# Kernel optimization log

Hardware: AMD Instinct MI355X
Metric: run time of the kernel (lower is better)

## Reference

```python
import jax, jax.numpy as jnp
import numpy as np

B, F, E = 1024, 1024, 256      # batch, flat_shape (mobilenet), embedding_size
L1, L2, L3 = 16, 8, 32         # level1 classes, level2 classes per branch, level3 classes per leaf
NE3 = L1 * L2                  # 128 leaf (level-3) classifier heads


def setup_inputs() -> dict:
    key = jax.random.key(0)
    ks = jax.random.split(key, 10)
    w = lambda k, shape: (jax.random.normal(k, shape, jnp.float32) * 0.02)
    return {
        "features_x": jax.random.normal(ks[0], (B, F), jnp.float32),
        "features_y": jax.random.normal(ks[1], (B, F), jnp.float32),
        # level-1 head: Linear(F->E, no bias) + LayerNorm + ReLU + Linear(E->L1)
        "l1_W1": w(ks[2], (F, E)),
        "l1_g": jnp.ones((E,), jnp.float32), "l1_b": jnp.zeros((E,), jnp.float32),
        "l1_W2": w(ks[3], (E, L1)), "l1_b2": jnp.zeros((L1,), jnp.float32),
        # level-2 heads (one per level-1 class), stacked on a leading expert axis
        "l2_W1": w(ks[4], (L1, F, E)),
        "l2_g": jnp.ones((L1, E), jnp.float32), "l2_b": jnp.zeros((L1, E), jnp.float32),
        "l2_W2": w(ks[5], (L1, E, L2)), "l2_b2": jnp.zeros((L1, L2), jnp.float32),
        # level-3 heads (flattened [level1][level2] -> NE3 experts)
        "l3_W1": w(ks[6], (NE3, F, E)),
        "l3_g": jnp.ones((NE3, E), jnp.float32), "l3_b": jnp.zeros((NE3, E), jnp.float32),
        "l3_W2": w(ks[7], (NE3, E, L3)), "l3_b2": jnp.zeros((NE3, L3), jnp.float32),
    }


def _ln(h, g, b, eps=1e-5):
    m = jnp.mean(h, axis=-1, keepdims=True)
    v = jnp.mean(jnp.square(h - m), axis=-1, keepdims=True)
    return (h - m) * jax.lax.rsqrt(v + eps) * g + b


def reference(features_x, features_y,
              l1_W1, l1_g, l1_b, l1_W2, l1_b2,
              l2_W1, l2_g, l2_b, l2_W2, l2_b2,
              l3_W1, l3_g, l3_b, l3_W2, l3_b2):
    # Dropout is identity in eval mode.
    x, y = features_x, features_y
    rows = jnp.arange(x.shape[0])

    # level 1: single head on x
    h1 = jax.nn.relu(_ln(x @ l1_W1, l1_g, l1_b))
    logits1 = h1 @ l1_W2 + l1_b2                                # [B, L1]
    idx1 = jnp.argmax(logits1, axis=-1)                         # argmax(softmax) == argmax

    # level 2: routed head on 0.6*x + 0.4*y; compute all L1 heads batched, gather selected
    ft = 0.6 * x + 0.4 * y
    h2 = jax.nn.relu(_ln(jnp.einsum('bf,efh->beh', ft, l2_W1), l2_g, l2_b))  # [B, L1, E]
    logits2_all = jnp.einsum('beh,ehc->bec', h2, l2_W2) + l2_b2              # [B, L1, L2]
    logits2 = logits2_all[rows, idx1]                                        # [B, L2]
    idx2 = jnp.argmax(logits2, axis=-1)

    # level 3: doubly-routed head on x; flat expert index = idx1*L2 + idx2
    eidx = idx1 * logits2.shape[-1] + idx2
    h3 = jax.nn.relu(_ln(jnp.einsum('bf,efh->beh', x, l3_W1), l3_g, l3_b))   # [B, NE3, E]
    logits3_all = jnp.einsum('beh,ehc->bec', h3, l3_W2) + l3_b2              # [B, NE3, L3]
    logits3 = logits3_all[rows, eidx]                                        # [B, L3]

    # uniform class counts => pad_sequence is a no-op
    return (logits1, logits2, logits3)
```

## Files before the change

### kernel.cpp

```cpp
#include <hip/hip_runtime.h>

#define B_    1024
#define F_    1024
#define E_    256
#define NL1   16
#define NL2   8
#define NL3   32
#define NE3_  128
#define CS1   4
#define CS    8
#define MAXCH2 160
#define MAXCH3 256
#define OUT2_OFF (B_ * NL1)
#define OUT3_OFF (B_ * (NL1 + NL2))

__device__ __forceinline__ float b2f(unsigned short u) {
    union { unsigned int i; float f; } v; v.i = ((unsigned int)u) << 16; return v.f;
}
__device__ __forceinline__ unsigned short f2b(float f) {
    union { float f; unsigned int i; } v; v.f = f;
    unsigned int x = v.i; x += 0x7fffu + ((x >> 16) & 1u);
    return (unsigned short)(x >> 16);
}

template<int R, int NC>
__device__ void head_chunk(
    const float* __restrict__ in,
    const void* W1v, const void* gv_, const void* bv_,
    const void* W2v, const void* b2v, int bf,
    float* part,
    float* hn,
    float* red,
    float* lg,
    int t)
{
    const int lane = t & 63;
    const int grp  = t >> 6;
    const int e0   = lane * 4;

    float acc[R][4];
    #pragma unroll
    for (int r = 0; r < R; ++r) { acc[r][0]=0.f; acc[r][1]=0.f; acc[r][2]=0.f; acc[r][3]=0.f; }

    const float* ing = in + grp * 256;

    if (bf) {
        const unsigned short* W = (const unsigned short*)W1v + (size_t)grp * 256 * E_;
        for (int f0 = 0; f0 < 256; f0 += 16) {
            ushort4 w[16];
            #pragma unroll
            for (int k = 0; k < 16; ++k)
                w[k] = *(const ushort4*)(W + (size_t)(f0 + k) * E_ + e0);
            #pragma unroll
            for (int q = 0; q < 4; ++q) {
                float4 xq[R];
                #pragma unroll
                for (int r = 0; r < R; ++r)
                    xq[r] = *(const float4*)(ing + r * F_ + f0 + q * 4);
                #pragma unroll
                for (int k2 = 0; k2 < 4; ++k2) {
                    ushort4 ww = w[q * 4 + k2];
                    float w0 = b2f(ww.x), w1 = b2f(ww.y), w2 = b2f(ww.z), w3 = b2f(ww.w);
                    #pragma unroll
                    for (int r = 0; r < R; ++r) {
                        float xv = (k2 == 0) ? xq[r].x : (k2 == 1) ? xq[r].y
                                 : (k2 == 2) ? xq[r].z : xq[r].w;
                        acc[r][0] += xv * w0; acc[r][1] += xv * w1;
                        acc[r][2] += xv * w2; acc[r][3] += xv * w3;
                    }
                }
            }
        }
    } else {
        const float* W = (const float*)W1v + (size_t)grp * 256 * E_;
        for (int f0 = 0; f0 < 256; f0 += 8) {
            float4 w[8];
            #pragma unroll
            for (int k = 0; k < 8; ++k)
                w[k] = *(const float4*)(W + (size_t)(f0 + k) * E_ + e0);
            #pragma unroll
            for (int q = 0; q < 2; ++q) {
                float4 xq[R];
                #pragma unroll
                for (int r = 0; r < R; ++r)
                    xq[r] = *(const float4*)(ing + r * F_ + f0 + q * 4);
                #pragma unroll
                for (int k2 = 0; k2 < 4; ++k2) {
                    float4 ww = w[q * 4 + k2];
                    #pragma unroll
                    for (int r = 0; r < R; ++r) {
                        float xv = (k2 == 0) ? xq[r].x : (k2 == 1) ? xq[r].y
                                 : (k2 == 2) ? xq[r].z : xq[r].w;
                        acc[r][0] += xv * ww.x; acc[r][1] += xv * ww.y;
                        acc[r][2] += xv * ww.z; acc[r][3] += xv * ww.w;
                    }
                }
            }
        }
    }

    #pragma unroll
    for (int r = 0; r < R; ++r) {
        part[(size_t)(grp * R + r) * E_ + e0 + 0] = acc[r][0];
        part[(size_t)(grp * R + r) * E_ + e0 + 1] = acc[r][1];
        part[(size_t)(grp * R + r) * E_ + e0 + 2] = acc[r][2];
        part[(size_t)(grp * R + r) * E_ + e0 + 3] = acc[r][3];
    }
    __syncthreads();

    float h[R];
    #pragma unroll
    for (int r = 0; r < R; ++r)
        h[r] = part[(0 * R + r) * E_ + t] + part[(1 * R + r) * E_ + t]
             + part[(2 * R + r) * E_ + t] + part[(3 * R + r) * E_ + t];

    #pragma unroll
    for (int r = 0; r < R; ++r) {
        float s = h[r], ss = h[r] * h[r];
        #pragma unroll
        for (int o = 32; o > 0; o >>= 1) { s += __shfl_xor(s, o); ss += __shfl_xor(ss, o); }
        if (lane == 0) { red[(grp * R + r) * 2 + 0] = s; red[(grp * R + r) * 2 + 1] = ss; }
    }
    __syncthreads();

    float gv, bv;
    if (bf) { gv = b2f(((const unsigned short*)gv_)[t]); bv = b2f(((const unsigned short*)bv_)[t]); }
    else    { gv = ((const float*)gv_)[t];               bv = ((const float*)bv_)[t]; }

    #pragma unroll
    for (int r = 0; r < R; ++r) {
        float S  = red[(0*R+r)*2] + red[(1*R+r)*2] + red[(2*R+r)*2] + red[(3*R+r)*2];
        float SS = red[(0*R+r)*2+1] + red[(1*R+r)*2+1] + red[(2*R+r)*2+1] + red[(3*R+r)*2+1];
        float m    = S * (1.0f / E_);
        float var  = SS * (1.0f / E_) - m * m;
        float rstd = rsqrtf(var + 1e-5f);
        hn[r * E_ + t] = fmaxf((h[r] - m) * rstd * gv + bv, 0.0f);
    }
    __syncthreads();

    constexpr int RN = R * NC;
    constexpr int G  = 256 / RN;
    constexpr int CH = E_ / G;
    const int oi = t % RN, j = t / RN, r = oi / NC, c = oi % NC;
    float a = 0.f;
    if (bf) {
        const unsigned short* W = (const unsigned short*)W2v;
        #pragma unroll 8
        for (int e = j * CH; e < j * CH + CH; ++e) a += hn[r * E_ + e] * b2f(W[(size_t)e * NC + c]);
    } else {
        const float* W = (const float*)W2v;
        #pragma unroll 8
        for (int e = j * CH; e < j * CH + CH; ++e) a += hn[r * E_ + e] * W[(size_t)e * NC + c];
    }
    float bias = bf ? b2f(((const unsigned short*)b2v)[c]) : ((const float*)b2v)[c];
    if (G > 1) {
        part[t] = a;
        __syncthreads();
        if (j == 0) {
            float sum = a;
            #pragma unroll
            for (int jj = 1; jj < G; ++jj) sum += part[jj * RN + oi];
            lg[oi] = sum + bias;
        }
    } else {
        lg[oi] = a + bias;
    }
    __syncthreads();
}

__global__ void dtype_sniff_kernel(const unsigned int* l1g_words, int* flag) {
    if (threadIdx.x == 0 && blockIdx.x == 0)
        *flag = (l1g_words[0] == 0x3F803F80u) ? 1 : 0;
}

__global__ __launch_bounds__(256) void mlc_level1_kernel(
    const void* x, const void* W1, const void* g, const void* b,
    const void* W2, const void* b2, void* out, int* idx1, const int* flagp)
{
    __shared__ float in_s[CS1 * F_];
    __shared__ float part[4 * CS1 * E_];
    __shared__ float hn[CS1 * E_];
    __shared__ float red[4 * CS1 * 2];
    __shared__ float lg[CS1 * NL1];

    const int t = threadIdx.x;
    const int bf = *flagp;
    const int row0 = blockIdx.x * CS1;

    #pragma unroll
    for (int r = 0; r < CS1; ++r) {
        if (bf) {
            ushort4 xv = ((const ushort4*)x)[(size_t)(row0 + r) * 256 + t];
            in_s[r * F_ + t*4+0] = b2f(xv.x); in_s[r * F_ + t*4+1] = b2f(xv.y);
            in_s[r * F_ + t*4+2] = b2f(xv.z); in_s[r * F_ + t*4+3] = b2f(xv.w);
        } else {
            float4 xv = ((const float4*)x)[(size_t)(row0 + r) * 256 + t];
            in_s[r * F_ + t*4+0] = xv.x; in_s[r * F_ + t*4+1] = xv.y;
            in_s[r * F_ + t*4+2] = xv.z; in_s[r * F_ + t*4+3] = xv.w;
        }
    }
    __syncthreads();

    head_chunk<CS1, NL1>(in_s, W1, g, b, W2, b2, bf, part, hn, red, lg, t);

    if (t < CS1 * NL1) {
        int r = t / NL1, c = t % NL1;
        size_t o = (size_t)(row0 + r) * NL1 + c;
        if (bf) ((unsigned short*)out)[o] = f2b(lg[t]);
        else    ((float*)out)[o] = lg[t];
        if (c == 0) {
            float best = lg[r * NL1]; int bi = 0;
            #pragma unroll
            for (int cc = 1; cc < NL1; ++cc)
                if (lg[r * NL1 + cc] > best) { best = lg[r * NL1 + cc]; bi = cc; }
            idx1[row0 + r] = bi;
        }
    }
}

template<int NEXP, int MAXCH>
__global__ __launch_bounds__(1024) void mlc_route_kernel(
    const int* __restrict__ src, int* __restrict__ rows_out, int4* __restrict__ chunks_out)
{
    __shared__ int hist[NEXP], offs[NEXP], cur[NEXP];
    const int t = threadIdx.x;
    if (t < NEXP) hist[t] = 0;
    __syncthreads();
    int e = src[t];
    if (e < 0) e = 0; if (e >= NEXP) e = NEXP - 1;
    atomicAdd(&hist[e], 1);
    __syncthreads();
    if (t == 0) {
        int o = 0;
        for (int i = 0; i < NEXP; ++i) { offs[i] = o; cur[i] = o; o += hist[i]; }
    }
    __syncthreads();
    int pos = atomicAdd(&cur[e], 1);
    if (pos >= 0 && pos < B_) rows_out[pos] = t;
    if (t == 0) {
        int nch = 0;
        for (int i = 0; i < NEXP; ++i) {
            int n = hist[i], st = offs[i];
            for (int j = 0; j < n && nch < MAXCH; j += CS)
                chunks_out[nch++] = make_int4(i, st + j, min(CS, n - j), 0);
        }
        for (; nch < MAXCH; ++nch) chunks_out[nch] = make_int4(0, 0, 0, 0);
    }
}

__global__ __launch_bounds__(256) void mlc_level2_kernel(
    const void* x, const void* y,
    const void* W1b, const void* gb, const void* bb,
    const void* W2b, const void* b2b,
    const int4* __restrict__ chunks, const int* __restrict__ rowlist,
    void* out, int* eidx, const int* flagp)
{
    __shared__ float in_s[CS * F_];
    __shared__ float part[4 * CS * E_];
    __shared__ float hn[CS * E_];
    __shared__ float red[4 * CS * 2];
    __shared__ float lg[CS * NL2];
    __shared__ int4  chs;
    __shared__ int   rows_s[CS];

    const int t = threadIdx.x;
    const int bf = *flagp;

    if (t == 0) chs = chunks[blockIdx.x];
    __syncthreads();
    const int expert = chs.x, start = chs.y, count = chs.z;
    if (count <= 0) return;
    if (t < CS) rows_s[t] = (t < count) ? rowlist[start + t] : -1;
    __syncthreads();

    #pragma unroll
    for (int r = 0; r < CS; ++r) {
        int row = rows_s[r];
        float f0 = 0.f, f1 = 0.f, f2 = 0.f, f3 = 0.f;
        if (row >= 0) {
            if (bf) {
                ushort4 xv = ((const ushort4*)x)[(size_t)row * 256 + t];
                ushort4 yv = ((const ushort4*)y)[(size_t)row * 256 + t];
                f0 = 0.6f * b2f(xv.x) + 0.4f * b2f(yv.x);
                f1 = 0.6f * b2f(xv.y) + 0.4f * b2f(yv.y);
                f2 = 0.6f * b2f(xv.z) + 0.4f * b2f(yv.z);
                f3 = 0.6f * b2f(xv.w) + 0.4f * b2f(yv.w);
            } else {
                float4 xv = ((const float4*)x)[(size_t)row * 256 + t];
                float4 yv = ((const float4*)y)[(size_t)row * 256 + t];
                f0 = 0.6f * xv.x + 0.4f * yv.x; f1 = 0.6f * xv.y + 0.4f * yv.y;
                f2 = 0.6f * xv.z + 0.4f * yv.z; f3 = 0.6f * xv.w + 0.4f * yv.w;
            }
        }
        in_s[r * F_ + t*4+0] = f0; in_s[r * F_ + t*4+1] = f1;
        in_s[r * F_ + t*4+2] = f2; in_s[r * F_ + t*4+3] = f3;
    }
    __syncthreads();

    const void* W1 = bf ? (const void*)((const unsigned short*)W1b + (size_t)expert * F_ * E_)
                        : (const void*)((const float*)W1b + (size_t)expert * F_ * E_);
    const void* g  = bf ? (const void*)((const unsigned short*)gb + (size_t)expert * E_)
                        : (const void*)((const float*)gb + (size_t)expert * E_);
    const void* b  = bf ? (const void*)((const unsigned short*)bb + (size_t)expert * E_)
                        : (const void*)((const float*)bb + (size_t)expert * E_);
    const void* W2 = bf ? (const void*)((const unsigned short*)W2b + (size_t)expert * E_ * NL2)
                        : (const void*)((const float*)W2b + (size_t)expert * E_ * NL2);
    const void* b2 = bf ? (const void*)((const unsigned short*)b2b + (size_t)expert * NL2)
                        : (const void*)((const float*)b2b + (size_t)expert * NL2);

    head_chunk<CS, NL2>(in_s, W1, g, b, W2, b2, bf, part, hn, red, lg, t);

    if (t < CS * NL2) {
        int r = t / NL2, c = t % NL2;
        if (r < count) {
            size_t o = (size_t)OUT2_OFF + (size_t)rows_s[r] * NL2 + c;
            if (bf) ((unsigned short*)out)[o] = f2b(lg[t]);
            else    ((float*)out)[o] = lg[t];
            if (c == 0) {
                float best = lg[r * NL2]; int bi = 0;
                #pragma unroll
                for (int cc = 1; cc < NL2; ++cc)
                    if (lg[r * NL2 + cc] > best) { best = lg[r * NL2 + cc]; bi = cc; }
                eidx[rows_s[r]] = expert * NL2 + bi;
            }
        }
    }
}

__global__ __launch_bounds__(256) void MultiLevelClassifier_26491358282059_kernel(
    const void* x,
    const void* W1b, const void* gb, const void* bb,
    const void* W2b, const void* b2b,
    const int4* __restrict__ chunks, const int* __restrict__ rowlist,
    void* out, const int* flagp)
{
    __shared__ float in_s[CS * F_];
    __shared__ float part[4 * CS * E_];
    __shared__ float hn[CS * E_];
    __shared__ float red[4 * CS * 2];
    __shared__ float lg[CS * NL3];
    __shared__ int4  chs;
    __shared__ int   rows_s[CS];

    const int t = threadIdx.x;
    const int bf = *flagp;

    if (t == 0) chs = chunks[blockIdx.x];
    __syncthreads();
    const int expert = chs.x, start = chs.y, count = chs.z;
    if (count <= 0) return;
    if (t < CS) rows_s[t] = (t < count) ? rowlist[start + t] : -1;
    __syncthreads();

    #pragma unroll
    for (int r = 0; r < CS; ++r) {
        int row = rows_s[r];
        float f0 = 0.f, f1 = 0.f, f2 = 0.f, f3 = 0.f;
        if (row >= 0) {
            if (bf) {
                ushort4 xv = ((const ushort4*)x)[(size_t)row * 256 + t];
                f0 = b2f(xv.x); f1 = b2f(xv.y); f2 = b2f(xv.z); f3 = b2f(xv.w);
            } else {
                float4 xv = ((const float4*)x)[(size_t)row * 256 + t];
                f0 = xv.x; f1 = xv.y; f2 = xv.z; f3 = xv.w;
            }
        }
        in_s[r * F_ + t*4+0] = f0; in_s[r * F_ + t*4+1] = f1;
        in_s[r * F_ + t*4+2] = f2; in_s[r * F_ + t*4+3] = f3;
    }
    __syncthreads();

    const void* W1 = bf ? (const void*)((const unsigned short*)W1b + (size_t)expert * F_ * E_)
                        : (const void*)((const float*)W1b + (size_t)expert * F_ * E_);
    const void* g  = bf ? (const void*)((const unsigned short*)gb + (size_t)expert * E_)
                        : (const void*)((const float*)gb + (size_t)expert * E_);
    const void* b  = bf ? (const void*)((const unsigned short*)bb + (size_t)expert * E_)
                        : (const void*)((const float*)bb + (size_t)expert * E_);
    const void* W2 = bf ? (const void*)((const unsigned short*)W2b + (size_t)expert * E_ * NL3)
                        : (const void*)((const float*)W2b + (size_t)expert * E_ * NL3);
    const void* b2 = bf ? (const void*)((const unsigned short*)b2b + (size_t)expert * NL3)
                        : (const void*)((const float*)b2b + (size_t)expert * NL3);

    head_chunk<CS, NL3>(in_s, W1, g, b, W2, b2, bf, part, hn, red, lg, t);

    if (t < CS * NL3) {
        int r = t / NL3, c = t % NL3;
        if (r < count) {
            size_t o = (size_t)OUT3_OFF + (size_t)rows_s[r] * NL3 + c;
            if (bf) ((unsigned short*)out)[o] = f2b(lg[t]);
            else    ((float*)out)[o] = lg[t];
        }
    }
}

extern "C" void kernel_launch(void* const* d_in, const int* in_sizes, int n_in,
                              void* d_out, int out_size, void* d_ws, size_t ws_size,
                              hipStream_t stream) {
    (void)in_sizes; (void)n_in; (void)out_size; (void)ws_size;

    int* ws = (int*)d_ws;
    int*  flag  = ws;
    int*  idx1  = ws + 64;
    int*  eidx  = ws + 1088;
    int*  rows2 = ws + 2112;
    int*  rows3 = ws + 3136;
    int4* ch2   = (int4*)(ws + 4160);
    int4* ch3   = (int4*)(ws + 4160 + MAXCH2 * 4);

    dtype_sniff_kernel<<<1, 1, 0, stream>>>((const unsigned int*)d_in[3], flag);

    mlc_level1_kernel<<<B_ / CS1, 256, 0, stream>>>(
        d_in[0], d_in[2], d_in[3], d_in[4], d_in[5], d_in[6],
        d_out, idx1, flag);

    mlc_route_kernel<NL1, MAXCH2><<<1, 1024, 0, stream>>>(idx1, rows2, ch2);

    mlc_level2_kernel<<<MAXCH2, 256, 0, stream>>>(
        d_in[0], d_in[1], d_in[7], d_in[8], d_in[9], d_in[10], d_in[11],
        ch2, rows2, d_out, eidx, flag);

    mlc_route_kernel<NE3_, MAXCH3><<<1, 1024, 0, stream>>>(eidx, rows3, ch3);

    MultiLevelClassifier_26491358282059_kernel<<<MAXCH3, 256, 0, stream>>>(
        d_in[0], d_in[12], d_in[13], d_in[14], d_in[15], d_in[16],
        ch3, rows3, d_out, flag);
}
```

Measured before the change: 344.6 us.

## Use bf16 MFMA for level-3 expert heads with 16-row chunks

Rewrites the level-3 routed head kernel to stage gathered input rows as bf16 in swizzled shared memory and compute the F->E projection with 16x16x32 bf16 MFMA instructions instead of scalar FMA. The chunk size for level-3 routing goes from 8 to 16 rows, so each expert's weights are read by fewer blocks, and a fused LayerNorm/ReLU plus a direct E->L3 dot loop replaces the generic head. The aim is to cut weight traffic and raise arithmetic throughput in the dominant level-3 stage. In exchange, fp32 inputs are rounded to bf16, which loses precision. The weight B-fragments are also loaded as strided scalar gathers, which may limit bandwidth.

```diff
diff --git a/kernel.cpp b/kernel.cpp
--- a/kernel.cpp
+++ b/kernel.cpp
@@ -1,4 +1,5 @@
 #include <hip/hip_runtime.h>
+
 
 #define B_    1024
 #define F_    1024
@@ -8,11 +9,15 @@
 #define NL3   32
 #define NE3_  128
 #define CS1   4
-#define CS    8
+#define CS2   8
+#define CS3   16
 #define MAXCH2 160
-#define MAXCH3 256
+#define MAXCH3 192
 #define OUT2_OFF (B_ * NL1)
 #define OUT3_OFF (B_ * (NL1 + NL2))
+
+typedef __attribute__((ext_vector_type(8))) short bf16x8_t;
+typedef __attribute__((ext_vector_type(4))) float f32x4_t;
 
 __device__ __forceinline__ float b2f(unsigned short u) {
     union { unsigned int i; float f; } v; v.i = ((unsigned int)u) << 16; return v.f;
@@ -28,11 +33,7 @@
     const float* __restrict__ in,
     const void* W1v, const void* gv_, const void* bv_,
     const void* W2v, const void* b2v, int bf,
-    float* part,
-    float* hn,
-    float* red,
-    float* lg,
-    int t)
+    float* part, float* hn, float* red, float* lg, int t)
 {
     const int lane = t & 63;
     const int grp  = t >> 6;
@@ -218,7 +219,7 @@
     }
 }
 
-template<int NEXP, int MAXCH>
+template<int NEXP, int MAXCH, int CHUNK>
 __global__ __launch_bounds__(1024) void mlc_route_kernel(
     const int* __restrict__ src, int* __restrict__ rows_out, int4* __restrict__ chunks_out)
 {
@@ -241,8 +242,8 @@
         int nch = 0;
         for (int i = 0; i < NEXP; ++i) {
             int n = hist[i], st = offs[i];
-            for (int j = 0; j < n && nch < MAXCH; j += CS)
-                chunks_out[nch++] = make_int4(i, st + j, min(CS, n - j), 0);
+            for (int j = 0; j < n && nch < MAXCH; j += CHUNK)
+                chunks_out[nch++] = make_int4(i, st + j, min(CHUNK, n - j), 0);
         }
         for (; nch < MAXCH; ++nch) chunks_out[nch] = make_int4(0, 0, 0, 0);
     }
@@ -255,13 +256,13 @@
     const int4* __restrict__ chunks, const int* __restrict__ rowlist,
     void* out, int* eidx, const int* flagp)
 {
-    __shared__ float in_s[CS * F_];
-    __shared__ float part[4 * CS * E_];
-    __shared__ float hn[CS * E_];
-    __shared__ float red[4 * CS * 2];
-    __shared__ float lg[CS * NL2];
+    __shared__ float in_s[CS2 * F_];
+    __shared__ float part[4 * CS2 * E_];
+    __shared__ float hn[CS2 * E_];
+    __shared__ float red[4 * CS2 * 2];
+    __shared__ float lg[CS2 * NL2];
     __shared__ int4  chs;
-    __shared__ int   rows_s[CS];
+    __shared__ int   rows_s[CS2];
 
     const int t = threadIdx.x;
     const int bf = *flagp;
@@ -270,11 +271,11 @@
     __syncthreads();
     const int expert = chs.x, start = chs.y, count = chs.z;
     if (count <= 0) return;
-    if (t < CS) rows_s[t] = (t < count) ? rowlist[start + t] : -1;
-    __syncthreads();
-
-    #pragma unroll
-    for (int r = 0; r < CS; ++r) {
+    if (t < CS2) rows_s[t] = (t < count) ? rowlist[start + t] : -1;
+    __syncthreads();
+
+    #pragma unroll
+    for (int r = 0; r < CS2; ++r) {
         int row = rows_s[r];
         float f0 = 0.f, f1 = 0.f, f2 = 0.f, f3 = 0.f;
         if (row >= 0) {
@@ -308,9 +309,9 @@
     const void* b2 = bf ? (const void*)((const unsigned short*)b2b + (size_t)expert * NL2)
                         : (const void*)((const float*)b2b + (size_t)expert * NL2);
 
-    head_chunk<CS, NL2>(in_s, W1, g, b, W2, b2, bf, part, hn, red, lg, t);
-
-    if (t < CS * NL2) {
+    head_chunk<CS2, NL2>(in_s, W1, g, b, W2, b2, bf, part, hn, red, lg, t);
+
+    if (t < CS2 * NL2) {
         int r = t / NL2, c = t % NL2;
         if (r < count) {
             size_t o = (size_t)OUT2_OFF + (size_t)rows_s[r] * NL2 + c;
@@ -327,6 +328,119 @@
     }
 }
 
+
+__device__ __forceinline__ void stage_rows(
+    unsigned short* xs, const void* xg, const int* rows, int bf, int t)
+{
+    const int r = t >> 4;
+    const int row = rows[r];
+    #pragma unroll
+    for (int i = 0; i < 8; ++i) {
+        const int c  = (t & 15) + 16 * i;
+        const int cs = c ^ (r & 7);
+        uint4 v = make_uint4(0u, 0u, 0u, 0u);
+        if (row >= 0) {
+            if (bf) {
+                v = *(const uint4*)((const unsigned short*)xg + (size_t)row * F_ + c * 8);
+            } else {
+                const float* xf = (const float*)xg + (size_t)row * F_ + c * 8;
+                float4 fa = *(const float4*)xf;
+                float4 fb = *(const float4*)(xf + 4);
+                v.x = ((unsigned)f2b(fa.y) << 16) | f2b(fa.x);
+                v.y = ((unsigned)f2b(fa.w) << 16) | f2b(fa.z);
+                v.z = ((unsigned)f2b(fb.y) << 16) | f2b(fb.x);
+                v.w = ((unsigned)f2b(fb.w) << 16) | f2b(fb.z);
+            }
+        }
+        *(uint4*)(xs + (size_t)r * F_ + cs * 8) = v;
+    }
+}
+
+__device__ void mfma_w1s(const unsigned short* xs, const void* W1v, int bf,
+                         float* h, int t)
+{
+    const int l    = t & 63;
+    const int w    = t >> 6;
+    const int u    = l >> 4;
+    const int row  = l & 15;
+    const int colb = w * 64 + row;
+
+    f32x4_t acc[4];
+    #pragma unroll
+    for (int tl = 0; tl < 4; ++tl) acc[tl] = (f32x4_t){0.f, 0.f, 0.f, 0.f};
+
+    if (bf) {
+        const unsigned short* __restrict__ W = (const unsigned short*)W1v;
+        for (int k0 = 0; k0 < F_; k0 += 32) {
+            const int cs = ((k0 >> 3) + u) ^ (row & 7);
+            bf16x8_t ax = *(const bf16x8_t*)(xs + (size_t)row * F_ + cs * 8);
+            const unsigned short* __restrict__ Wk = W + (size_t)(k0 + u * 8) * E_ + colb;
+            #pragma unroll
+            for (int tl = 0; tl < 4; ++tl) {
+                bf16x8_t b;
+                #pragma unroll
+                for (int e = 0; e < 8; ++e) b[e] = (short)Wk[e * E_ + tl * 16];
+                acc[tl] = __builtin_amdgcn_mfma_f32_16x16x32_bf16(ax, b, acc[tl], 0, 0, 0);
+            }
+        }
+    } else {
+        const float* __restrict__ W = (const float*)W1v;
+        for (int k0 = 0; k0 < F_; k0 += 32) {
+            const int cs = ((k0 >> 3) + u) ^ (row & 7);
+            bf16x8_t ax = *(const bf16x8_t*)(xs + (size_t)row * F_ + cs * 8);
+            const float* __restrict__ Wk = W + (size_t)(k0 + u * 8) * E_ + colb;
+            #pragma unroll
+            for (int tl = 0; tl < 4; ++tl) {
+                bf16x8_t b;
+                #pragma unroll
+                for (int e = 0; e < 8; ++e) b[e] = (short)f2b(Wk[e * E_ + tl * 16]);
+                acc[tl] = __builtin_amdgcn_mfma_f32_16x16x32_bf16(ax, b, acc[tl], 0, 0, 0);
+            }
+        }
+    }
+
+    #pragma unroll
+    for (int tl = 0; tl < 4; ++tl) {
+        #pragma unroll
+        for (int j = 0; j < 4; ++j)
+            h[(size_t)(u * 4 + j) * E_ + colb + tl * 16] = acc[tl][j];
+    }
+}
+
+__device__ void ln_relu16(float* h, const void* g_, const void* b_,
+                          int bf, int t, float* red)
+{
+    __syncthreads();
+    const int l = t & 63, w = t >> 6;
+    float hv[16];
+    #pragma unroll
+    for (int r = 0; r < 16; ++r) hv[r] = h[(size_t)r * E_ + t];
+
+    #pragma unroll
+    for (int r = 0; r < 16; ++r) {
+        float s = hv[r], ss = hv[r] * hv[r];
+        #pragma unroll
+        for (int o = 32; o > 0; o >>= 1) { s += __shfl_xor(s, o); ss += __shfl_xor(ss, o); }
+        if (l == 0) { red[(w * 16 + r) * 2] = s; red[(w * 16 + r) * 2 + 1] = ss; }
+    }
+    __syncthreads();
+
+    float gv, bv;
+    if (bf) { gv = b2f(((const unsigned short*)g_)[t]); bv = b2f(((const unsigned short*)b_)[t]); }
+    else    { gv = ((const float*)g_)[t];               bv = ((const float*)b_)[t]; }
+
+    #pragma unroll
+    for (int r = 0; r < 16; ++r) {
+        float S  = red[r * 2]     + red[(16 + r) * 2]     + red[(32 + r) * 2]     + red[(48 + r) * 2];
+        float SS = red[r * 2 + 1] + red[(16 + r) * 2 + 1] + red[(32 + r) * 2 + 1] + red[(48 + r) * 2 + 1];
+        float m    = S * (1.0f / E_);
+        float var  = SS * (1.0f / E_) - m * m;
+        float rstd = rsqrtf(var + 1e-5f);
+        h[(size_t)r * E_ + t] = fmaxf((hv[r] - m) * rstd * gv + bv, 0.0f);
+    }
+    __syncthreads();
+}
+
 __global__ __launch_bounds__(256) void MultiLevelClassifier_26491358282059_kernel(
     const void* x,
     const void* W1b, const void* gb, const void* bb,
@@ -334,40 +448,23 @@
     const int4* __restrict__ chunks, const int* __restrict__ rowlist,
     void* out, const int* flagp)
 {
-    __shared__ float in_s[CS * F_];
-    __shared__ float part[4 * CS * E_];
-    __shared__ float hn[CS * E_];
-    __shared__ float red[4 * CS * 2];
-    __shared__ float lg[CS * NL3];
+    __shared__ __align__(16) unsigned short xs[16 * F_];
+    __shared__ float h[16 * E_];
+    __shared__ float red[128];
     __shared__ int4  chs;
-    __shared__ int   rows_s[CS];
-
-    const int t = threadIdx.x;
+    __shared__ int   rows_s[16];
+
+    const int t  = threadIdx.x;
     const int bf = *flagp;
 
     if (t == 0) chs = chunks[blockIdx.x];
     __syncthreads();
     const int expert = chs.x, start = chs.y, count = chs.z;
     if (count <= 0) return;
-    if (t < CS) rows_s[t] = (t < count) ? rowlist[start + t] : -1;
-    __syncthreads();
-
-    #pragma unroll
-    for (int r = 0; r < CS; ++r) {
-        int row = rows_s[r];
-        float f0 = 0.f, f1 = 0.f, f2 = 0.f, f3 = 0.f;
-        if (row >= 0) {
-            if (bf) {
-                ushort4 xv = ((const ushort4*)x)[(size_t)row * 256 + t];
-                f0 = b2f(xv.x); f1 = b2f(xv.y); f2 = b2f(xv.z); f3 = b2f(xv.w);
-            } else {
-                float4 xv = ((const float4*)x)[(size_t)row * 256 + t];
-                f0 = xv.x; f1 = xv.y; f2 = xv.z; f3 = xv.w;
-            }
-        }
-        in_s[r * F_ + t*4+0] = f0; in_s[r * F_ + t*4+1] = f1;
-        in_s[r * F_ + t*4+2] = f2; in_s[r * F_ + t*4+3] = f3;
-    }
+    if (t < 16) rows_s[t] = (t < count) ? rowlist[start + t] : -1;
+    __syncthreads();
+
+    stage_rows(xs, x, rows_s, bf, t);
     __syncthreads();
 
     const void* W1 = bf ? (const void*)((const unsigned short*)W1b + (size_t)expert * F_ * E_)
@@ -381,14 +478,41 @@
     const void* b2 = bf ? (const void*)((const unsigned short*)b2b + (size_t)expert * NL3)
                         : (const void*)((const float*)b2b + (size_t)expert * NL3);
 
-    head_chunk<CS, NL3>(in_s, W1, g, b, W2, b2, bf, part, hn, red, lg, t);
-
-    if (t < CS * NL3) {
-        int r = t / NL3, c = t % NL3;
+    mfma_w1s(xs, W1, bf, h, t);
+    ln_relu16(h, g, b, bf, t, red);
+
+    {
+        const int r = t >> 4, c0 = t & 15;
+        float a0 = 0.f, a1 = 0.f;
+        if (bf) {
+            const unsigned short* W = (const unsigned short*)W2;
+            #pragma unroll 4
+            for (int e = 0; e < E_; ++e) {
+                float hv = h[(size_t)r * E_ + e];
+                a0 += hv * b2f(W[(size_t)e * NL3 + c0]);
+                a1 += hv * b2f(W[(size_t)e * NL3 + c0 + 16]);
+            }
+        } else {
+            const float* W = (const float*)W2;
+            #pragma unroll 4
+            for (int e = 0; e < E_; ++e) {
+                float hv = h[(size_t)r * E_ + e];
+                a0 += hv * W[(size_t)e * NL3 + c0];
+                a1 += hv * W[(size_t)e * NL3 + c0 + 16];
+            }
+        }
         if (r < count) {
-            size_t o = (size_t)OUT3_OFF + (size_t)rows_s[r] * NL3 + c;
-            if (bf) ((unsigned short*)out)[o] = f2b(lg[t]);
-            else    ((float*)out)[o] = lg[t];
+            float bb0, bb1;
+            if (bf) { bb0 = b2f(((const unsigned short*)b2)[c0]); bb1 = b2f(((const unsigned short*)b2)[c0 + 16]); }
+            else    { bb0 = ((const float*)b2)[c0];               bb1 = ((const float*)b2)[c0 + 16]; }
+            size_t o = (size_t)OUT3_OFF + (size_t)rows_s[r] * NL3 + c0;
+            if (bf) {
+                ((unsigned short*)out)[o]      = f2b(a0 + bb0);
+                ((unsigned short*)out)[o + 16] = f2b(a1 + bb1);
+            } else {
+                ((float*)out)[o]      = a0 + bb0;
+                ((float*)out)[o + 16] = a1 + bb1;
+            }
         }
     }
 }
@@ -405,7 +529,7 @@
     int*  rows2 = ws + 2112;
     int*  rows3 = ws + 3136;
     int4* ch2   = (int4*)(ws + 4160);
-    int4* ch3   = (int4*)(ws + 4160 + MAXCH2 * 4);
+    int4* ch3   = (int4*)(ws + 4800);
 
     dtype_sniff_kernel<<<1, 1, 0, stream>>>((const unsigned int*)d_in[3], flag);
 
@@ -413,13 +537,13 @@
         d_in[0], d_in[2], d_in[3], d_in[4], d_in[5], d_in[6],
         d_out, idx1, flag);
 
-    mlc_route_kernel<NL1, MAXCH2><<<1, 1024, 0, stream>>>(idx1, rows2, ch2);
+    mlc_route_kernel<NL1, MAXCH2, CS2><<<1, 1024, 0, stream>>>(idx1, rows2, ch2);
 
     mlc_level2_kernel<<<MAXCH2, 256, 0, stream>>>(
         d_in[0], d_in[1], d_in[7], d_in[8], d_in[9], d_in[10], d_in[11],
         ch2, rows2, d_out, eidx, flag);
 
-    mlc_route_kernel<NE3_, MAXCH3><<<1, 1024, 0, stream>>>(eidx, rows3, ch3);
+    mlc_route_kernel<NE3_, MAXCH3, CS3><<<1, 1024, 0, stream>>>(eidx, rows3, ch3);
 
     MultiLevelClassifier_26491358282059_kernel<<<MAXCH3, 256, 0, stream>>>(
         d_in[0], d_in[12], d_in[13], d_in[14], d_in[15], d_in[16],
```

Result: slower. 360.6 us (+4.6%).
